# Optimization experiments

Measured on AMD Instinct MI355X. Metric: run time of the kernel, lower is better.

The kernel has to match this reference:

```python
import jax, jax.numpy as jnp
import numpy as np
from jax.scipy.ndimage import map_coordinates

B, G, C, H, W = 8, 16, 1, 384, 384
K = 3                    # rectangular (box) kernel size
KV = float(K * K)        # kernel volume (sum of ones kernel)
LBD = 1.0
SMOOTH_DR = 1e-5         # monai LNCC default smooth_dr (smooth_nr = 0)


def setup_inputs() -> dict:
    key = jax.random.key(0)
    k1, k2 = jax.random.split(key)
    images = jax.random.normal(k1, (B, G, C, H, W), dtype=jnp.float32)
    warps = jax.random.normal(k2, (B, G, 2, H, W), dtype=jnp.float32)
    return {"images": images, "warps": warps}


def _warp2d(images, flow):
    """Bilinear warp. images [N,C,H,W], flow [N,2,H,W] (pixel displacements,
    channel 0 = x/width, channel 1 = y/height). Border-clamped sampling."""
    gy, gx = jnp.meshgrid(jnp.arange(H, dtype=images.dtype),
                          jnp.arange(W, dtype=images.dtype), indexing="ij")
    cy = gy[None] + flow[:, 1]   # [N,H,W]
    cx = gx[None] + flow[:, 0]   # [N,H,W]

    def samp(img2d, cy_, cx_):
        return map_coordinates(img2d, [cy_, cx_], order=1, mode="nearest")

    # vmap over channels, then over batch
    per_img = jax.vmap(samp, in_axes=(0, None, None))        # over C
    return jax.vmap(per_img, in_axes=(0, 0, 0))(images, cy, cx)  # over N


def _box_sum(x):
    """3x3 box-filter sum with zero padding (SAME). x: [N,C,H,W]."""
    k = jnp.ones((1, 1, K, K), x.dtype)
    return jax.lax.conv_general_dilated(
        x, k, window_strides=(1, 1), padding="SAME",
        dimension_numbers=("NCHW", "OIHW", "NCHW"))


def _lncc_loss(pred, target):
    """monai LocalNormalizedCrossCorrelationLoss (rectangular kernel)."""
    t_sum = _box_sum(target)
    p_sum = _box_sum(pred)
    t2_sum = _box_sum(target * target)
    p2_sum = _box_sum(pred * pred)
    tp_sum = _box_sum(target * pred)
    t_avg = t_sum / KV
    p_avg = p_sum / KV
    cross = tp_sum - p_avg * t_sum
    t_var = jnp.maximum(t2_sum - t_avg * t_sum, 0.0)
    p_var = jnp.maximum(p2_sum - p_avg * p_sum, 0.0)
    ncc = (cross * cross) / (t_var * p_var + SMOOTH_DR)
    return -jnp.mean(ncc)


def reference(images, warps):
    imgs = images.reshape(B * G, C, H, W)
    flow = warps.reshape(B * G, 2, H, W)
    warped = _warp2d(imgs, flow)                       # [B*G,C,H,W]
    template = jnp.mean(warped, axis=0, keepdims=True)  # [1,C,H,W]
    lncc = _lncc_loss(jnp.broadcast_to(template, warped.shape), warped)
    # Grad2d('l2') on warps [B,G,2,H,W]
    dy = warps[:, :, :, 1:, :] - warps[:, :, :, :-1, :]
    dx = warps[:, :, :, :, 1:] - warps[:, :, :, :, :-1]
    g2 = (jnp.mean(dx * dx) + jnp.mean(dy * dy)) / 2.0
    return lncc + LBD * g2
```

## Files before the change

### kernel.cpp

```cpp
#include <hip/hip_runtime.h>
#include <hip/hip_fp16.h>

#define HH 384
#define WW 384
#define HW (HH * WW)
#define NIMG 128
#define NPIX (NIMG * HW)
#define GRAD_CNT 37650432.0

#define K1_TH 8
#define K1_M  4
#define K1_NT (HH / K1_TH)
#define K1_SROWS (K1_TH + 2 * K1_M)
#define K1_LSH 432
#define NP_G (K1_NT * NIMG)

#define K2_SPLIT 8

#define K3_T 32
#define K3_NX (WW / K3_T)
#define K3_TILES (K3_NX * (HH / K3_T))
#define NP_N (K3_TILES * NIMG)

__device__ inline int pad_off(int x) { return x + 4 * (x >> 5); }

__device__ inline void block_reduce_store_256(float v, float* dst) {
    #pragma unroll
    for (int o = 32; o > 0; o >>= 1) v += __shfl_down(v, o);
    __shared__ float s[4];
    int wave = threadIdx.x >> 6, lane = threadIdx.x & 63;
    if (lane == 0) s[wave] = v;
    __syncthreads();
    if (threadIdx.x == 0) *dst = s[0] + s[1] + s[2] + s[3];
}

__global__ __launch_bounds__(256, 8) void warp_grad_kernel(
        const float* __restrict__ images, const float* __restrict__ warps,
        __half* __restrict__ warped, float* __restrict__ partialsG) {
    __shared__ __half simg[K1_SROWS * K1_LSH];
    int n = blockIdx.y;
    int yt = blockIdx.x;
    int y0 = yt * K1_TH;
    int ys0 = max(0, y0 - K1_M);
    int ys1 = min(HH - 1, y0 + K1_TH - 1 + K1_M);
    int cnt = ys1 - ys0 + 1;
    const float* img = images + (size_t)n * HW;
    int tid = threadIdx.x;

    for (int i = tid; i < cnt * 96; i += 256) {
        int r = i / 96, gg = i - r * 96;
        int x0 = gg * 4;
        float4 v = *(const float4*)(img + (ys0 + r) * WW + x0);
        union { __half2 h2[2]; uint2 u; } pk;
        pk.h2[0] = __floats2half2_rn(v.x, v.y);
        pk.h2[1] = __floats2half2_rn(v.z, v.w);
        *(uint2*)(simg + r * K1_LSH + pad_off(x0)) = pk.u;
    }
    __syncthreads();

    const float* flow0 = warps + (size_t)n * 2 * HW;
    const float* flow1 = flow0 + HW;
    float g = 0.f;

    #pragma unroll
    for (int gi = 0; gi < 3; ++gi) {
        int p4 = gi * 256 + tid;
        int r = p4 / 96;
        int c4 = p4 - r * 96;
        int x0 = c4 * 4;
        int y = y0 + r;
        int base = y * WW + x0;

        float4 f0 = *(const float4*)(flow0 + base);
        float4 f1 = *(const float4*)(flow1 + base);

        float d;
        d = f0.y - f0.x; g += d * d;  d = f1.y - f1.x; g += d * d;
        d = f0.z - f0.y; g += d * d;  d = f1.z - f1.y; g += d * d;
        d = f0.w - f0.z; g += d * d;  d = f1.w - f1.z; g += d * d;
        if (x0 + 4 < WW) {
            float a0 = flow0[base + 4], a1 = flow1[base + 4];
            d = a0 - f0.w; g += d * d;  d = a1 - f1.w; g += d * d;
        }
        if (y + 1 < HH) {
            float4 b0 = *(const float4*)(flow0 + base + WW);
            float4 b1 = *(const float4*)(flow1 + base + WW);
            d = b0.x - f0.x; g += d * d;  d = b1.x - f1.x; g += d * d;
            d = b0.y - f0.y; g += d * d;  d = b1.y - f1.y; g += d * d;
            d = b0.z - f0.z; g += d * d;  d = b1.z - f1.z; g += d * d;
            d = b0.w - f0.w; g += d * d;  d = b1.w - f1.w; g += d * d;
        }

        float fxa[4] = {f0.x, f0.y, f0.z, f0.w};
        float fya[4] = {f1.x, f1.y, f1.z, f1.w};
        float o[4];
        #pragma unroll
        for (int j = 0; j < 4; ++j) {
            float cx = (float)(x0 + j) + fxa[j];
            float cy = (float)y + fya[j];
            float flx = floorf(cx), fly = floorf(cy);
            float wx = cx - flx, wy = cy - fly;
            int xi = (int)flx, yi = (int)fly;
            int x0c = min(max(xi, 0), WW - 1), x1c = min(max(xi + 1, 0), WW - 1);
            int y0c = min(max(yi, 0), HH - 1), y1c = min(max(yi + 1, 0), HH - 1);
            float v00, v01, v10, v11;
            if (y0c >= ys0 && y1c <= ys1) {
                const __half* r0 = simg + (y0c - ys0) * K1_LSH;
                const __half* r1 = simg + (y1c - ys0) * K1_LSH;
                int oa = pad_off(x0c), ob = pad_off(x1c);
                v00 = __half2float(r0[oa]); v01 = __half2float(r0[ob]);
                v10 = __half2float(r1[oa]); v11 = __half2float(r1[ob]);
            } else {
                v00 = img[y0c * WW + x0c]; v01 = img[y0c * WW + x1c];
                v10 = img[y1c * WW + x0c]; v11 = img[y1c * WW + x1c];
            }
            float top = v00 + wx * (v01 - v00);
            float bot = v10 + wx * (v11 - v10);
            o[j] = top + wy * (bot - top);
        }
        union { __half2 h2[2]; uint2 u; } cv;
        cv.h2[0] = __floats2half2_rn(o[0], o[1]);
        cv.h2[1] = __floats2half2_rn(o[2], o[3]);
        *(uint2*)(warped + (size_t)n * HW + base) = cv.u;
    }
    block_reduce_store_256(g, &partialsG[(size_t)n * K1_NT + yt]);
}

__global__ __launch_bounds__(256) void template_part_kernel(
        const __half* __restrict__ warped, float* __restrict__ tpart) {
    int p8 = blockIdx.x * 256 + threadIdx.x;
    int q = blockIdx.y;
    const __half* p = warped + (size_t)q * (NIMG / K2_SPLIT) * HW + p8 * 8;
    float s[8] = {0, 0, 0, 0, 0, 0, 0, 0};
    #pragma unroll 4
    for (int nn = 0; nn < NIMG / K2_SPLIT; ++nn) {
        union { uint4 u; __half2 h2[4]; } cv;
        cv.u = *(const uint4*)(p + (size_t)nn * HW);
        #pragma unroll
        for (int k = 0; k < 4; ++k) {
            float2 f = __half22float2(cv.h2[k]);
            s[2 * k] += f.x; s[2 * k + 1] += f.y;
        }
    }
    float* dst = tpart + (size_t)q * HW + p8 * 8;
    *(float4*)dst       = make_float4(s[0], s[1], s[2], s[3]);
    *(float4*)(dst + 4) = make_float4(s[4], s[5], s[6], s[7]);
}

__global__ __launch_bounds__(256) void template_combine_kernel(
        const float* __restrict__ tpart, float* __restrict__ templ) {
    int p4 = blockIdx.x * 256 + threadIdx.x;
    float sx = 0, sy = 0, sz = 0, sw = 0;
    #pragma unroll
    for (int pl = 0; pl < K2_SPLIT; ++pl) {
        float4 a = *(const float4*)(tpart + (size_t)pl * HW + p4 * 4);
        sx += a.x; sy += a.y; sz += a.z; sw += a.w;
    }
    const float sc = 1.f / (float)NIMG;
    *(float4*)(templ + p4 * 4) = make_float4(sx * sc, sy * sc, sz * sc, sw * sc);
}

__global__ __launch_bounds__(256) void lncc_kernel(
        const __half* __restrict__ warped, const float* __restrict__ templ,
        float* __restrict__ partialsN) {
    __shared__ float st[34][40];
    __shared__ float sp[34][40];
    int n = blockIdx.y;
    int tile = blockIdx.x;
    int tyt = tile / K3_NX, txt = tile - tyt * K3_NX;
    int oy0 = tyt * K3_T, ox0 = txt * K3_T;
    const __half* t = warped + (size_t)n * HW;
    int tid = threadIdx.x;

    for (int i = tid; i < 34 * 10; i += 256) {
        int ly = i / 10, c = i - (i / 10) * 10;
        int gy = oy0 + ly - 1;
        int gx = ox0 - 4 + c * 4;
        float4 tv = {0.f, 0.f, 0.f, 0.f}, pv = {0.f, 0.f, 0.f, 0.f};
        if (gy >= 0 && gy < HH && gx >= 0 && gx + 3 < WW) {
            union { uint2 u; __half2 h2[2]; } cv;
            cv.u = *(const uint2*)(t + gy * WW + gx);
            float2 lo = __half22float2(cv.h2[0]);
            float2 hi = __half22float2(cv.h2[1]);
            tv = make_float4(lo.x, lo.y, hi.x, hi.y);
            pv = *(const float4*)(templ + gy * WW + gx);
        }
        *(float4*)&st[ly][c * 4] = tv;
        *(float4*)&sp[ly][c * 4] = pv;
    }
    __syncthreads();

    int tx = tid & 7, ty = tid >> 3;
    int xb = tx * 4;
    float cT[6] = {0,0,0,0,0,0}, cP[6] = {0,0,0,0,0,0};
    float cT2[6] = {0,0,0,0,0,0}, cP2[6] = {0,0,0,0,0,0}, cTP[6] = {0,0,0,0,0,0};
    #pragma unroll
    for (int r = 0; r < 3; ++r) {
        float t0 = st[ty + r][xb + 3];
        float4 t4 = *(const float4*)&st[ty + r][xb + 4];
        float t5 = st[ty + r][xb + 8];
        float p0 = sp[ty + r][xb + 3];
        float4 p4 = *(const float4*)&sp[ty + r][xb + 4];
        float p5 = sp[ty + r][xb + 8];
        float tv[6] = {t0, t4.x, t4.y, t4.z, t4.w, t5};
        float pv[6] = {p0, p4.x, p4.y, p4.z, p4.w, p5};
        #pragma unroll
        for (int c = 0; c < 6; ++c) {
            cT[c] += tv[c]; cP[c] += pv[c];
            cT2[c] = fmaf(tv[c], tv[c], cT2[c]);
            cP2[c] = fmaf(pv[c], pv[c], cP2[c]);
            cTP[c] = fmaf(tv[c], pv[c], cTP[c]);
        }
    }
    const float inv9 = 1.f / 9.f;
    float nccsum = 0.f;
    #pragma unroll
    for (int j = 0; j < 4; ++j) {
        float ts = cT[j] + cT[j + 1] + cT[j + 2];
        float ps = cP[j] + cP[j + 1] + cP[j + 2];
        float t2s = cT2[j] + cT2[j + 1] + cT2[j + 2];
        float p2s = cP2[j] + cP2[j + 1] + cP2[j + 2];
        float tps = cTP[j] + cTP[j + 1] + cTP[j + 2];
        float cross = tps - (ps * inv9) * ts;
        float tvar = fmaxf(t2s - (ts * inv9) * ts, 0.f);
        float pvar = fmaxf(p2s - (ps * inv9) * ps, 0.f);
        nccsum += (cross * cross) / (tvar * pvar + 1e-5f);
    }
    block_reduce_store_256(nccsum, &partialsN[(size_t)n * K3_TILES + tile]);
}

__global__ __launch_bounds__(1024) void finalize_kernel(
        const float* __restrict__ pN, const float* __restrict__ pG,
        float* __restrict__ out) {
    double accN = 0.0, accG = 0.0;
    for (int i = threadIdx.x; i < NP_N; i += 1024) accN += (double)pN[i];
    for (int i = threadIdx.x; i < NP_G; i += 1024) accG += (double)pG[i];
    #pragma unroll
    for (int o = 32; o > 0; o >>= 1) {
        accN += __shfl_down(accN, o);
        accG += __shfl_down(accG, o);
    }
    __shared__ double sN[16], sG[16];
    int wave = threadIdx.x >> 6, lane = threadIdx.x & 63;
    if (lane == 0) { sN[wave] = accN; sG[wave] = accG; }
    __syncthreads();
    if (threadIdx.x == 0) {
        double tN = 0.0, tG = 0.0;
        #pragma unroll
        for (int w = 0; w < 16; ++w) { tN += sN[w]; tG += sG[w]; }
        double lncc = -(tN / (double)NPIX);
        double g2 = tG / (2.0 * GRAD_CNT);
        out[0] = (float)(lncc + g2);
    }
}

extern "C" void kernel_launch(void* const* d_in, const int* in_sizes, int n_in,
                              void* d_out, int out_size, void* d_ws, size_t ws_size,
                              hipStream_t stream) {
    const float* images = (const float*)d_in[0];
    const float* warps  = (const float*)d_in[1];
    float* out = (float*)d_out;

    __half* warped  = (__half*)d_ws;
    float* fbase    = (float*)((char*)d_ws + (size_t)NPIX * 2);
    float* partialsN = fbase;
    float* partialsG = partialsN + NP_N;
    float* tpart     = partialsG + NP_G;
    float* templ     = tpart + (size_t)K2_SPLIT * HW;

    warp_grad_kernel<<<dim3(K1_NT, NIMG), dim3(256), 0, stream>>>(
        images, warps, warped, partialsG);
    template_part_kernel<<<dim3(HW / 8 / 256, K2_SPLIT), dim3(256), 0, stream>>>(
        warped, tpart);
    template_combine_kernel<<<dim3(HW / 4 / 256), dim3(256), 0, stream>>>(
        tpart, templ);
    lncc_kernel<<<dim3(K3_TILES, NIMG), dim3(256), 0, stream>>>(
        warped, templ, partialsN);
    finalize_kernel<<<dim3(1), dim3(1024), 0, stream>>>(
        partialsN, partialsG, out);
}
```

Measured before the change: 128.2 us.

## Enlarge warp tiles, shuffle right-neighbor flow, process two images per LNCC block

The warp kernel now covers 16 rows per block instead of 8, which halves the redundant halo loads of the image tile. The right-neighbor flow value for the x-gradient now comes from a lane shuffle, so each lane no longer does its own scalar global load. The LNCC kernel handles two images per block that share one template tile, which halves template loads and launches half as many blocks. The costs are more registers and LDS per block, lower occupancy bounds, and fewer blocks for the GPU to spread the work across.

```diff
diff --git a/kernel.cpp b/kernel.cpp
--- a/kernel.cpp
+++ b/kernel.cpp
@@ -8,7 +8,7 @@
 #define NPIX (NIMG * HW)
 #define GRAD_CNT 37650432.0
 
-#define K1_TH 8
+#define K1_TH 16
 #define K1_M  4
 #define K1_NT (HH / K1_TH)
 #define K1_SROWS (K1_TH + 2 * K1_M)
@@ -34,7 +34,24 @@
     if (threadIdx.x == 0) *dst = s[0] + s[1] + s[2] + s[3];
 }
 
-__global__ __launch_bounds__(256, 8) void warp_grad_kernel(
+__device__ inline void block_reduce_store2_256(float v0, float v1,
+                                               float* d0, float* d1) {
+    #pragma unroll
+    for (int o = 32; o > 0; o >>= 1) {
+        v0 += __shfl_down(v0, o);
+        v1 += __shfl_down(v1, o);
+    }
+    __shared__ float s0[4], s1[4];
+    int wave = threadIdx.x >> 6, lane = threadIdx.x & 63;
+    if (lane == 0) { s0[wave] = v0; s1[wave] = v1; }
+    __syncthreads();
+    if (threadIdx.x == 0) {
+        *d0 = s0[0] + s0[1] + s0[2] + s0[3];
+        *d1 = s1[0] + s1[1] + s1[2] + s1[3];
+    }
+}
+
+__global__ __launch_bounds__(256, 7) void warp_grad_kernel(
         const float* __restrict__ images, const float* __restrict__ warps,
         __half* __restrict__ warped, float* __restrict__ partialsG) {
     __shared__ __half simg[K1_SROWS * K1_LSH];
@@ -62,8 +79,8 @@
     const float* flow1 = flow0 + HW;
     float g = 0.f;
 
-    #pragma unroll
-    for (int gi = 0; gi < 3; ++gi) {
+    #pragma unroll 2
+    for (int gi = 0; gi < 6; ++gi) {
         int p4 = gi * 256 + tid;
         int r = p4 / 96;
         int c4 = p4 - r * 96;
@@ -74,14 +91,19 @@
         float4 f0 = *(const float4*)(flow0 + base);
         float4 f1 = *(const float4*)(flow1 + base);
 
+        float a0 = __shfl_down(f0.x, 1);
+        float a1 = __shfl_down(f1.x, 1);
+        if (c4 == 95) {
+            a0 = f0.w; a1 = f1.w;
+        } else if ((tid & 63) == 63) {
+            a0 = flow0[base + 4]; a1 = flow1[base + 4];
+        }
+
         float d;
         d = f0.y - f0.x; g += d * d;  d = f1.y - f1.x; g += d * d;
         d = f0.z - f0.y; g += d * d;  d = f1.z - f1.y; g += d * d;
         d = f0.w - f0.z; g += d * d;  d = f1.w - f1.z; g += d * d;
-        if (x0 + 4 < WW) {
-            float a0 = flow0[base + 4], a1 = flow1[base + 4];
-            d = a0 - f0.w; g += d * d;  d = a1 - f1.w; g += d * d;
-        }
+        d = a0 - f0.w;   g += d * d;  d = a1 - f1.w;   g += d * d;
         if (y + 1 < HH) {
             float4 b0 = *(const float4*)(flow0 + base + WW);
             float4 b1 = *(const float4*)(flow1 + base + WW);
@@ -163,70 +185,97 @@
 __global__ __launch_bounds__(256) void lncc_kernel(
         const __half* __restrict__ warped, const float* __restrict__ templ,
         float* __restrict__ partialsN) {
-    __shared__ float st[34][40];
+    __shared__ float st0[34][40];
+    __shared__ float st1[34][40];
     __shared__ float sp[34][40];
-    int n = blockIdx.y;
+    int n0 = blockIdx.y;
+    int n1 = n0 + 64;
     int tile = blockIdx.x;
     int tyt = tile / K3_NX, txt = tile - tyt * K3_NX;
     int oy0 = tyt * K3_T, ox0 = txt * K3_T;
-    const __half* t = warped + (size_t)n * HW;
+    const __half* t0 = warped + (size_t)n0 * HW;
+    const __half* t1 = warped + (size_t)n1 * HW;
     int tid = threadIdx.x;
 
     for (int i = tid; i < 34 * 10; i += 256) {
         int ly = i / 10, c = i - (i / 10) * 10;
         int gy = oy0 + ly - 1;
         int gx = ox0 - 4 + c * 4;
-        float4 tv = {0.f, 0.f, 0.f, 0.f}, pv = {0.f, 0.f, 0.f, 0.f};
+        float4 tv0 = {0, 0, 0, 0}, tv1 = {0, 0, 0, 0}, pv = {0, 0, 0, 0};
         if (gy >= 0 && gy < HH && gx >= 0 && gx + 3 < WW) {
             union { uint2 u; __half2 h2[2]; } cv;
-            cv.u = *(const uint2*)(t + gy * WW + gx);
+            cv.u = *(const uint2*)(t0 + gy * WW + gx);
             float2 lo = __half22float2(cv.h2[0]);
             float2 hi = __half22float2(cv.h2[1]);
-            tv = make_float4(lo.x, lo.y, hi.x, hi.y);
+            tv0 = make_float4(lo.x, lo.y, hi.x, hi.y);
+            cv.u = *(const uint2*)(t1 + gy * WW + gx);
+            lo = __half22float2(cv.h2[0]);
+            hi = __half22float2(cv.h2[1]);
+            tv1 = make_float4(lo.x, lo.y, hi.x, hi.y);
             pv = *(const float4*)(templ + gy * WW + gx);
         }
-        *(float4*)&st[ly][c * 4] = tv;
+        *(float4*)&st0[ly][c * 4] = tv0;
+        *(float4*)&st1[ly][c * 4] = tv1;
         *(float4*)&sp[ly][c * 4] = pv;
     }
     __syncthreads();
 
     int tx = tid & 7, ty = tid >> 3;
     int xb = tx * 4;
-    float cT[6] = {0,0,0,0,0,0}, cP[6] = {0,0,0,0,0,0};
-    float cT2[6] = {0,0,0,0,0,0}, cP2[6] = {0,0,0,0,0,0}, cTP[6] = {0,0,0,0,0,0};
+    float cA[6] = {0,0,0,0,0,0}, cA2[6] = {0,0,0,0,0,0}, cAP[6] = {0,0,0,0,0,0};
+    float cB[6] = {0,0,0,0,0,0}, cB2[6] = {0,0,0,0,0,0}, cBP[6] = {0,0,0,0,0,0};
+    float cP[6] = {0,0,0,0,0,0}, cP2[6] = {0,0,0,0,0,0};
     #pragma unroll
     for (int r = 0; r < 3; ++r) {
-        float t0 = st[ty + r][xb + 3];
-        float4 t4 = *(const float4*)&st[ty + r][xb + 4];
-        float t5 = st[ty + r][xb + 8];
+        float ta0 = st0[ty + r][xb + 3];
+        float4 ta4 = *(const float4*)&st0[ty + r][xb + 4];
+        float ta5 = st0[ty + r][xb + 8];
+        float tb0 = st1[ty + r][xb + 3];
+        float4 tb4 = *(const float4*)&st1[ty + r][xb + 4];
+        float tb5 = st1[ty + r][xb + 8];
         float p0 = sp[ty + r][xb + 3];
         float4 p4 = *(const float4*)&sp[ty + r][xb + 4];
         float p5 = sp[ty + r][xb + 8];
-        float tv[6] = {t0, t4.x, t4.y, t4.z, t4.w, t5};
+        float av[6] = {ta0, ta4.x, ta4.y, ta4.z, ta4.w, ta5};
+        float bv[6] = {tb0, tb4.x, tb4.y, tb4.z, tb4.w, tb5};
         float pv[6] = {p0, p4.x, p4.y, p4.z, p4.w, p5};
         #pragma unroll
         for (int c = 0; c < 6; ++c) {
-            cT[c] += tv[c]; cP[c] += pv[c];
-            cT2[c] = fmaf(tv[c], tv[c], cT2[c]);
+            cA[c] += av[c]; cB[c] += bv[c]; cP[c] += pv[c];
+            cA2[c] = fmaf(av[c], av[c], cA2[c]);
+            cB2[c] = fmaf(bv[c], bv[c], cB2[c]);
             cP2[c] = fmaf(pv[c], pv[c], cP2[c]);
-            cTP[c] = fmaf(tv[c], pv[c], cTP[c]);
+            cAP[c] = fmaf(av[c], pv[c], cAP[c]);
+            cBP[c] = fmaf(bv[c], pv[c], cBP[c]);
         }
     }
     const float inv9 = 1.f / 9.f;
-    float nccsum = 0.f;
+    float ncc0 = 0.f, ncc1 = 0.f;
     #pragma unroll
     for (int j = 0; j < 4; ++j) {
-        float ts = cT[j] + cT[j + 1] + cT[j + 2];
         float ps = cP[j] + cP[j + 1] + cP[j + 2];
-        float t2s = cT2[j] + cT2[j + 1] + cT2[j + 2];
         float p2s = cP2[j] + cP2[j + 1] + cP2[j + 2];
-        float tps = cTP[j] + cTP[j + 1] + cTP[j + 2];
-        float cross = tps - (ps * inv9) * ts;
-        float tvar = fmaxf(t2s - (ts * inv9) * ts, 0.f);
         float pvar = fmaxf(p2s - (ps * inv9) * ps, 0.f);
-        nccsum += (cross * cross) / (tvar * pvar + 1e-5f);
-    }
-    block_reduce_store_256(nccsum, &partialsN[(size_t)n * K3_TILES + tile]);
+        {
+            float ts = cA[j] + cA[j + 1] + cA[j + 2];
+            float t2s = cA2[j] + cA2[j + 1] + cA2[j + 2];
+            float tps = cAP[j] + cAP[j + 1] + cAP[j + 2];
+            float cross = tps - (ps * inv9) * ts;
+            float tvar = fmaxf(t2s - (ts * inv9) * ts, 0.f);
+            ncc0 += (cross * cross) / (tvar * pvar + 1e-5f);
+        }
+        {
+            float ts = cB[j] + cB[j + 1] + cB[j + 2];
+            float t2s = cB2[j] + cB2[j + 1] + cB2[j + 2];
+            float tps = cBP[j] + cBP[j + 1] + cBP[j + 2];
+            float cross = tps - (ps * inv9) * ts;
+            float tvar = fmaxf(t2s - (ts * inv9) * ts, 0.f);
+            ncc1 += (cross * cross) / (tvar * pvar + 1e-5f);
+        }
+    }
+    block_reduce_store2_256(ncc0, ncc1,
+                            &partialsN[(size_t)n0 * K3_TILES + tile],
+                            &partialsN[(size_t)n1 * K3_TILES + tile]);
 }
 
 __global__ __launch_bounds__(1024) void finalize_kernel(
@@ -274,7 +323,7 @@
         warped, tpart);
     template_combine_kernel<<<dim3(HW / 4 / 256), dim3(256), 0, stream>>>(
         tpart, templ);
-    lncc_kernel<<<dim3(K3_TILES, NIMG), dim3(256), 0, stream>>>(
+    lncc_kernel<<<dim3(K3_TILES, 64), dim3(256), 0, stream>>>(
         warped, templ, partialsN);
     finalize_kernel<<<dim3(1), dim3(1024), 0, stream>>>(
         partialsN, partialsG, out);
```

Measured after the change: 115.2 us. -10.2%, faster.
